# Kernel tuning notes

Hardware: AMD Instinct MI355X
Metric: run time of the kernel (lower is better)

The kernel has to match this reference:

```python
import jax, jax.numpy as jnp
import numpy as np

D_OUT, D1, D2 = 512, 512, 512
R0, R1, R2 = 128, 128, 128
BATCH = 8192


def setup_inputs() -> dict:
    key = jax.random.key(0)
    k1, k2, k3, k4, k5, k6 = jax.random.split(key, 6)
    return {
        "X1": jax.random.normal(k1, (D1, BATCH), dtype=jnp.float32),
        "X2": jax.random.normal(k2, (D2, BATCH), dtype=jnp.float32),
        "U0": jax.random.normal(k3, (D_OUT, R0), dtype=jnp.float32) * 0.05,
        "U1": jax.random.normal(k4, (D1, R1), dtype=jnp.float32) * 0.05,
        "U2": jax.random.normal(k5, (D2, R2), dtype=jnp.float32) * 0.05,
        "G": jax.random.normal(k6, (R0, R1, R2), dtype=jnp.float32) * 0.05,
    }


def reference(X1, X2, U0, U1, U2, G):
    # Per-mode projections: UX_i = U_{i+1}^T @ X_i  -> [r_i, B]
    UX1 = U1.T @ X1  # [R1, B]
    UX2 = U2.T @ X2  # [R2, B]
    # Column-wise Khatri-Rao product of UX1, UX2 gives kron per column with
    # row index q*R2 + r (C order), which matches mode-0 unfolding of G.
    # Fused form: core = G_(0) @ khatri_rao(UX1, UX2), expressed as one einsum.
    core = jnp.einsum('pqr,qb,rb->pb', G, UX1, UX2)  # [R0, B]
    Z = U0 @ core  # [D_OUT, B]
    return Z
```

## Files before the change

### kernel.cpp

```cpp
#include <hip/hip_runtime.h>
#include <hip/hip_bf16.h>
#include <stdint.h>


typedef __attribute__((ext_vector_type(8))) short bf8;
typedef __attribute__((ext_vector_type(4))) short bf4;
typedef __attribute__((ext_vector_type(4))) float f4;

__device__ __forceinline__ unsigned short f2bf(float f){
  unsigned x = __builtin_bit_cast(unsigned, f);
  x += 0x7fffu + ((x >> 16) & 1u);
  return (unsigned short)(x >> 16);
}
__device__ __forceinline__ float bf2f(unsigned short u){
  unsigned x = ((unsigned)u) << 16;
  return __builtin_bit_cast(float, x);
}
__device__ __forceinline__ void glds16(const void* g, void* l){
  __builtin_amdgcn_global_load_lds(
      (const __attribute__((address_space(1))) void*)g,
      (__attribute__((address_space(3))) void*)l, 16, 0, 0);
}

__global__ __launch_bounds__(256) void k_cast(const float* __restrict__ G,
                                              const float* __restrict__ U0,
                                              const float* __restrict__ U1,
                                              const float* __restrict__ U2,
                                              unsigned short* __restrict__ Gbf,
                                              unsigned short* __restrict__ U0bf,
                                              unsigned short* __restrict__ U1T,
                                              unsigned short* __restrict__ U2T){
  const int blk = blockIdx.x;
  if (blk < 2112){
    const int i4 = blk * 256 + threadIdx.x;
    const int NG4 = 2097152 / 4;
    const float4* src; unsigned short* dst; int j4;
    if (i4 < NG4){ src = (const float4*)G;  dst = Gbf;  j4 = i4; }
    else         { src = (const float4*)U0; dst = U0bf; j4 = i4 - NG4; }
    float4 v = src[j4];
    ushort4 o = make_ushort4(f2bf(v.x), f2bf(v.y), f2bf(v.z), f2bf(v.w));
    ((ushort4*)dst)[j4] = o;
  } else {
    const int b2 = blk - 2112;
    const float* U = (b2 < 256) ? U1 : U2;
    unsigned short* UT = (b2 < 256) ? U1T : U2T;
    const int idx = (b2 & 255) * 256 + threadIdx.x;
    const int d = idx >> 7, q = idx & 127;
    UT[q * 512 + d] = f2bf(U[idx]);
  }
}

__global__ __launch_bounds__(256) void k_ux2(const unsigned short* __restrict__ U1T,
                                             const unsigned short* __restrict__ U2T,
                                             const float* __restrict__ X1,
                                             const float* __restrict__ X2,
                                             float* __restrict__ OUTF,
                                             unsigned short* __restrict__ OUTT){
  const bool second = (blockIdx.y != 0);
  const unsigned short* UT = second ? U2T : U1T;
  const float* X = second ? X2 : X1;
  __shared__ __align__(16) unsigned char lds[16384 + 8192];
  unsigned char* ldsA = lds;
  unsigned char* ldsB = lds + 16384;
  const int tid = threadIdx.x, lane = tid & 63, wv = tid >> 6;
  const int wr = wv >> 1, wc = wv & 1;
  const int b0 = blockIdx.x * 64;
  f4 acc[4][2] = {};

  for (int it = 0; it < 8; ++it){
    const int k0 = it * 64;
#pragma unroll
    for (int i = 0; i < 4; ++i){
      const int L = (wv * 4 + i) * 1024 + lane * 16;
      const int row = L >> 7;
      const int ss = (lane & 7) ^ (row & 7);
      glds16(UT + (size_t)row * 512 + k0 + ss * 8, ldsA + (wv * 4 + i) * 1024);
    }
#pragma unroll
    for (int c = 0; c < 2; ++c){
      const int slot = c * 4 + wv;
      const int bRow = lane;
      bf8 v;
#pragma unroll
      for (int j = 0; j < 8; ++j)
        v[j] = (short)f2bf(X[(size_t)(k0 + slot * 8 + j) * 8192 + b0 + bRow]);
      *(bf8*)(ldsB + bRow * 128 + ((slot ^ (bRow & 7)) << 4)) = v;
    }
    __syncthreads();
#pragma unroll
    for (int kc = 0; kc < 2; ++kc){
      const int g = lane >> 4;
      bf8 a[4], b[2];
#pragma unroll
      for (int mf = 0; mf < 4; ++mf){
        const int r = wr * 64 + mf * 16 + (lane & 15);
        a[mf] = *(const bf8*)(ldsA + r * 128 + (((kc * 4 + g) ^ (r & 7)) << 4));
      }
#pragma unroll
      for (int nf = 0; nf < 2; ++nf){
        const int rb = wc * 32 + nf * 16 + (lane & 15);
        b[nf] = *(const bf8*)(ldsB + rb * 128 + (((kc * 4 + g) ^ (rb & 7)) << 4));
      }
#pragma unroll
      for (int mf = 0; mf < 4; ++mf)
#pragma unroll
        for (int nf = 0; nf < 2; ++nf)
          acc[mf][nf] = __builtin_amdgcn_mfma_f32_16x16x32_bf16(a[mf], b[nf], acc[mf][nf], 0, 0, 0);
    }
    __syncthreads();
  }

  if (!second){
#pragma unroll
    for (int mf = 0; mf < 4; ++mf)
#pragma unroll
      for (int nf = 0; nf < 2; ++nf)
#pragma unroll
        for (int j = 0; j < 4; ++j){
          const int q = wr * 64 + mf * 16 + (lane >> 4) * 4 + j;
          const int b = b0 + wc * 32 + nf * 16 + (lane & 15);
          OUTF[(size_t)q * 8192 + b] = acc[mf][nf][j];
        }
  } else {
#pragma unroll
    for (int mf = 0; mf < 4; ++mf)
#pragma unroll
      for (int nf = 0; nf < 2; ++nf){
        const int rBase = wr * 64 + mf * 16 + (lane >> 4) * 4;
        const int bL = wc * 32 + nf * 16 + (lane & 15);
        bf4 p;
#pragma unroll
        for (int j = 0; j < 4; ++j) p[j] = (short)f2bf(acc[mf][nf][j]);
        *(bf4*)(lds + ((bL * 256 + rBase * 2) ^ ((bL & 7) << 4))) = p;
      }
    __syncthreads();
#pragma unroll
    for (int u = 0; u < 4; ++u){
      const int sIdx = u * 256 + tid;
      const int bL = sIdx >> 4, slot = sIdx & 15;
      bf8 v = *(const bf8*)(lds + bL * 256 + ((slot ^ (bL & 7)) << 4));
      *(bf8*)(OUTT + (size_t)(b0 + bL) * 128 + slot * 8) = v;
    }
  }
}

__global__ __launch_bounds__(512, 2) void k_core(const unsigned short* __restrict__ Gbf,
                                                 const float* __restrict__ UX1,
                                                 const unsigned short* __restrict__ UX2T,
                                                 unsigned short* __restrict__ PT){
  __shared__ __align__(16) unsigned char lds[114688];
  unsigned char* ldsX = lds + 98304;
  const int tid = threadIdx.x, lane = tid & 63, wv = tid >> 6;
  const int g = lane >> 4, l15 = lane & 15;
  const int wr = wv >> 2, wc = wv & 3;
  const int blk = blockIdx.x;
  const int split = blk & 7;
  const int b0 = (blk >> 3) * 256;
  const int q0 = split * 16;

  auto stageA = [&](int q, int buf){
#pragma unroll
    for (int rnd = 0; rnd < 4; ++rnd){
      const int off = rnd * 8192 + wv * 1024 + lane * 16;
      const int row = off >> 8;
      const int ss = ((off >> 4) & 15) ^ (row & 7);
      glds16(Gbf + (size_t)row * 16384 + (size_t)q * 128 + ss * 8,
             lds + buf * 32768 + off);
    }
  };

  bf8 Bf[4][4];
#pragma unroll
  for (int kc = 0; kc < 4; ++kc)
#pragma unroll
    for (int nf = 0; nf < 4; ++nf)
      Bf[kc][nf] = *(const bf8*)(UX2T + (size_t)(b0 + wc * 64 + nf * 16 + l15) * 128 +
                                 kc * 32 + g * 8);
#pragma unroll
  for (int rnd = 0; rnd < 2; ++rnd){
    const int off = rnd * 8192 + wv * 1024 + lane * 16;
    const int row = off >> 10;
    glds16(UX1 + (size_t)(q0 + row) * 8192 + b0 + ((off >> 2) & 255), ldsX + off);
  }
  stageA(q0 + 0, 0);
  stageA(q0 + 1, 1);

  f4 acc[4][4];
#pragma unroll
  for (int mf = 0; mf < 4; ++mf)
#pragma unroll
    for (int nf = 0; nf < 4; ++nf) acc[mf][nf] = (f4){0.f, 0.f, 0.f, 0.f};

  int cur = 0;
  for (int i = 0; i < 16; ++i){
    if (i < 15) asm volatile("s_waitcnt vmcnt(4)" ::: "memory");
    else        asm volatile("s_waitcnt vmcnt(0)" ::: "memory");
    __builtin_amdgcn_s_barrier();
    if (i < 14){
      int sbuf = cur + 2; if (sbuf >= 3) sbuf -= 3;
      stageA(q0 + i + 2, sbuf);
    }

    const unsigned char* A = lds + cur * 32768;
    float xs[4];
#pragma unroll
    for (int nf = 0; nf < 4; ++nf)
      xs[nf] = *(const float*)(ldsX + i * 1024 + (wc * 64 + nf * 16 + l15) * 4);
#pragma unroll
    for (int mf = 0; mf < 4; ++mf){
      const int row = wr * 64 + mf * 16 + l15;
      bf8 a[4];
#pragma unroll
      for (int kc = 0; kc < 4; ++kc)
        a[kc] = *(const bf8*)(A + row * 256 + ((((kc << 2) + g) ^ (row & 7)) << 4));
#pragma unroll
      for (int nf = 0; nf < 4; ++nf){
        f4 y = __builtin_amdgcn_mfma_f32_16x16x32_bf16(a[0], Bf[0][nf], (f4){0.f,0.f,0.f,0.f}, 0, 0, 0);
        y = __builtin_amdgcn_mfma_f32_16x16x32_bf16(a[1], Bf[1][nf], y, 0, 0, 0);
        y = __builtin_amdgcn_mfma_f32_16x16x32_bf16(a[2], Bf[2][nf], y, 0, 0, 0);
        y = __builtin_amdgcn_mfma_f32_16x16x32_bf16(a[3], Bf[3][nf], y, 0, 0, 0);
        acc[mf][nf] += y * xs[nf];
      }
    }
    ++cur; if (cur == 3) cur = 0;
  }

  __syncthreads();
#pragma unroll
  for (int mf = 0; mf < 4; ++mf)
#pragma unroll
    for (int nf = 0; nf < 4; ++nf){
      const int bL = wc * 64 + nf * 16 + l15;
      const int pq = wr * 16 + mf * 4 + g;
      bf4 o;
#pragma unroll
      for (int j = 0; j < 4; ++j) o[j] = (short)f2bf(acc[mf][nf][j]);
      *(bf4*)(lds + bL * 256 + ((pq ^ (bL & 7)) << 3)) = o;
    }
  __syncthreads();
#pragma unroll
  for (int rnd = 0; rnd < 8; ++rnd){
    const int idx = rnd * 512 + tid;
    const int bL = idx >> 4, s8 = idx & 15;
    bf4 lo = *(const bf4*)(lds + bL * 256 + (((s8 * 2) ^ (bL & 7)) << 3));
    bf4 hi = *(const bf4*)(lds + bL * 256 + (((s8 * 2 + 1) ^ (bL & 7)) << 3));
    bf8 o;
#pragma unroll
    for (int j = 0; j < 4; ++j){ o[j] = lo[j]; o[4 + j] = hi[j]; }
    *(bf8*)(PT + (size_t)split * 1048576 + (size_t)(b0 + bL) * 128 + s8 * 8) = o;
  }
}

__global__ __launch_bounds__(256) void k_red(const unsigned short* __restrict__ PT,
                                             unsigned short* __restrict__ coreT){
  const int c = blockIdx.x * 256 + threadIdx.x;
  const bf8* P = (const bf8*)PT;
  float s[8] = {};
#pragma unroll
  for (int sp = 0; sp < 8; ++sp){
    bf8 v = P[c + sp * 131072];
#pragma unroll
    for (int j = 0; j < 8; ++j) s[j] += bf2f((unsigned short)v[j]);
  }
  bf8 o;
#pragma unroll
  for (int j = 0; j < 8; ++j) o[j] = (short)f2bf(s[j]);
  ((bf8*)coreT)[c] = o;
}

__global__ __launch_bounds__(256) void k_z(const unsigned short* __restrict__ U0bf,
                                           const unsigned short* __restrict__ coreT,
                                           float* __restrict__ Z){
  __shared__ __align__(16) unsigned char lds[32768];
  unsigned char* ldsA = lds;
  unsigned char* ldsB = lds + 16384;
  const int tid = threadIdx.x, lane = tid & 63, wv = tid >> 6;
  const int wr = wv >> 1, wc = wv & 1;
  const int b0 = blockIdx.x * 128;
  const int d0 = blockIdx.y * 128;
  f4 acc[4][4] = {};

#pragma unroll
  for (int it = 0; it < 2; ++it){
    const int k0 = it * 64;
#pragma unroll
    for (int i = 0; i < 4; ++i){
      const int L = (wv * 4 + i) * 1024 + lane * 16;
      const int row = L >> 7;
      const int ss = (lane & 7) ^ (row & 7);
      glds16(U0bf + (size_t)(d0 + row) * 128 + k0 + ss * 8, ldsA + (wv * 4 + i) * 1024);
      glds16(coreT + (size_t)(b0 + row) * 128 + k0 + ss * 8, ldsB + (wv * 4 + i) * 1024);
    }
    __syncthreads();
#pragma unroll
    for (int kc = 0; kc < 2; ++kc){
      const int g = lane >> 4;
      bf8 a[4], b[4];
#pragma unroll
      for (int mf = 0; mf < 4; ++mf){
        const int r = wr * 64 + mf * 16 + (lane & 15);
        a[mf] = *(const bf8*)(ldsA + r * 128 + (((kc * 4 + g) ^ (r & 7)) << 4));
      }
#pragma unroll
      for (int nf = 0; nf < 4; ++nf){
        const int rb = wc * 64 + nf * 16 + (lane & 15);
        b[nf] = *(const bf8*)(ldsB + rb * 128 + (((kc * 4 + g) ^ (rb & 7)) << 4));
      }
#pragma unroll
      for (int mf = 0; mf < 4; ++mf)
#pragma unroll
        for (int nf = 0; nf < 4; ++nf)
          acc[mf][nf] = __builtin_amdgcn_mfma_f32_16x16x32_bf16(a[mf], b[nf], acc[mf][nf], 0, 0, 0);
    }
    __syncthreads();
  }
#pragma unroll
  for (int mf = 0; mf < 4; ++mf)
#pragma unroll
    for (int nf = 0; nf < 4; ++nf)
#pragma unroll
      for (int j = 0; j < 4; ++j){
        const int d = d0 + wr * 64 + mf * 16 + (lane >> 4) * 4 + j;
        const int b = b0 + wc * 64 + nf * 16 + (lane & 15);
        Z[(size_t)d * 8192 + b] = acc[mf][nf][j];
      }
}

extern "C" void kernel_launch(void* const* d_in, const int* in_sizes, int n_in,
                              void* d_out, int out_size, void* d_ws, size_t ws_size,
                              hipStream_t stream){
  const float* X1 = (const float*)d_in[0];
  const float* X2 = (const float*)d_in[1];
  const float* U0 = (const float*)d_in[2];
  const float* U1 = (const float*)d_in[3];
  const float* U2 = (const float*)d_in[4];
  const float* G  = (const float*)d_in[5];
  float* Z = (float*)d_out;

  char* ws = (char*)d_ws;
  unsigned short* Gbf   = (unsigned short*)(ws);
  unsigned short* U0bf  = (unsigned short*)(ws + 4194304);
  unsigned short* U1T   = (unsigned short*)(ws + 4325376);
  unsigned short* U2T   = (unsigned short*)(ws + 4456448);
  float*          UX1   = (float*)         (ws + 4587520);
  unsigned short* UX2T  = (unsigned short*)(ws + 8781824);
  unsigned short* coreT = (unsigned short*)(ws + 10878976);
  unsigned short* PT    = (unsigned short*)(ws + 12976128);

  k_cast<<<dim3(2624), dim3(256), 0, stream>>>(G, U0, U1, U2, Gbf, U0bf, U1T, U2T);
  k_ux2 <<<dim3(128, 2), dim3(256), 0, stream>>>(U1T, U2T, X1, X2, UX1, UX2T);
  k_core<<<dim3(256), dim3(512), 0, stream>>>(Gbf, UX1, UX2T, PT);
  k_red <<<dim3(512), dim3(256), 0, stream>>>(PT, coreT);
  k_z   <<<dim3(64, 4), dim3(256), 0, stream>>>(U0bf, coreT, Z);
}
```

Measured before the change: 69.11 us.

## Split k_core into smaller blocks with double-buffered G staging and direct stores

k_core now launches 1024 blocks of 256 threads instead of 256 blocks of 512. Each block covers 64 rows of p and 128 batch columns, which cuts LDS use to 32KB and allows more blocks per CU. The triple-buffered pipeline with manual vmcnt waits becomes a simple double buffer with __syncthreads. UX1 scalars are read straight from global memory rather than staged in LDS, and results go directly to PT as 8-byte stores without the LDS transpose. The trade-offs are less latency hiding, more redundant UX2T loads across blocks, and narrower, less coalesced output writes.

```diff
diff --git a/kernel.cpp b/kernel.cpp
--- a/kernel.cpp
+++ b/kernel.cpp
@@ -144,28 +144,31 @@
   }
 }
 
-__global__ __launch_bounds__(512, 2) void k_core(const unsigned short* __restrict__ Gbf,
+__global__ __launch_bounds__(256, 3) void k_core(const unsigned short* __restrict__ Gbf,
                                                  const float* __restrict__ UX1,
                                                  const unsigned short* __restrict__ UX2T,
                                                  unsigned short* __restrict__ PT){
-  __shared__ __align__(16) unsigned char lds[114688];
-  unsigned char* ldsX = lds + 98304;
-  const int tid = threadIdx.x, lane = tid & 63, wv = tid >> 6;
+  __shared__ __align__(16) unsigned char lds[32768];
+  const int tid = threadIdx.x, lane = tid & 63;
+  const int wv = tid >> 6;
   const int g = lane >> 4, l15 = lane & 15;
-  const int wr = wv >> 2, wc = wv & 3;
+  const int wr = wv >> 1, wc = wv & 1;
   const int blk = blockIdx.x;
   const int split = blk & 7;
-  const int b0 = (blk >> 3) * 256;
+  const int rest = blk >> 3;
+  const int pt = (rest & 1) * 64;
+  const int b0 = (rest >> 1) * 128;
   const int q0 = split * 16;
 
   auto stageA = [&](int q, int buf){
 #pragma unroll
     for (int rnd = 0; rnd < 4; ++rnd){
-      const int off = rnd * 8192 + wv * 1024 + lane * 16;
+      const int off = rnd * 4096 + tid * 16;
       const int row = off >> 8;
-      const int ss = ((off >> 4) & 15) ^ (row & 7);
-      glds16(Gbf + (size_t)row * 16384 + (size_t)q * 128 + ss * 8,
-             lds + buf * 32768 + off);
+      const int slot = (off >> 4) & 15;
+      const int ss = slot ^ (row & 15);
+      glds16(Gbf + (size_t)(pt + row) * 16384 + (size_t)q * 128 + ss * 8,
+             lds + buf * 16384 + off);
     }
   };
 
@@ -176,43 +179,30 @@
     for (int nf = 0; nf < 4; ++nf)
       Bf[kc][nf] = *(const bf8*)(UX2T + (size_t)(b0 + wc * 64 + nf * 16 + l15) * 128 +
                                  kc * 32 + g * 8);
-#pragma unroll
-  for (int rnd = 0; rnd < 2; ++rnd){
-    const int off = rnd * 8192 + wv * 1024 + lane * 16;
-    const int row = off >> 10;
-    glds16(UX1 + (size_t)(q0 + row) * 8192 + b0 + ((off >> 2) & 255), ldsX + off);
-  }
-  stageA(q0 + 0, 0);
-  stageA(q0 + 1, 1);
-
-  f4 acc[4][4];
-#pragma unroll
-  for (int mf = 0; mf < 4; ++mf)
+  stageA(q0, 0);
+
+  f4 acc[2][4];
+#pragma unroll
+  for (int mf = 0; mf < 2; ++mf)
 #pragma unroll
     for (int nf = 0; nf < 4; ++nf) acc[mf][nf] = (f4){0.f, 0.f, 0.f, 0.f};
 
-  int cur = 0;
   for (int i = 0; i < 16; ++i){
-    if (i < 15) asm volatile("s_waitcnt vmcnt(4)" ::: "memory");
-    else        asm volatile("s_waitcnt vmcnt(0)" ::: "memory");
-    __builtin_amdgcn_s_barrier();
-    if (i < 14){
-      int sbuf = cur + 2; if (sbuf >= 3) sbuf -= 3;
-      stageA(q0 + i + 2, sbuf);
-    }
-
-    const unsigned char* A = lds + cur * 32768;
+    __syncthreads();
+    if (i < 15) stageA(q0 + i + 1, (i + 1) & 1);
+
+    const unsigned char* A = lds + (i & 1) * 16384;
     float xs[4];
 #pragma unroll
     for (int nf = 0; nf < 4; ++nf)
-      xs[nf] = *(const float*)(ldsX + i * 1024 + (wc * 64 + nf * 16 + l15) * 4);
-#pragma unroll
-    for (int mf = 0; mf < 4; ++mf){
-      const int row = wr * 64 + mf * 16 + l15;
+      xs[nf] = UX1[(size_t)(q0 + i) * 8192 + b0 + wc * 64 + nf * 16 + l15];
+#pragma unroll
+    for (int mf = 0; mf < 2; ++mf){
+      const int row = wr * 32 + mf * 16 + l15;
       bf8 a[4];
 #pragma unroll
       for (int kc = 0; kc < 4; ++kc)
-        a[kc] = *(const bf8*)(A + row * 256 + ((((kc << 2) + g) ^ (row & 7)) << 4));
+        a[kc] = *(const bf8*)(A + row * 256 + ((((kc << 2) + g) ^ l15) << 4));
 #pragma unroll
       for (int nf = 0; nf < 4; ++nf){
         f4 y = __builtin_amdgcn_mfma_f32_16x16x32_bf16(a[0], Bf[0][nf], (f4){0.f,0.f,0.f,0.f}, 0, 0, 0);
@@ -222,33 +212,18 @@
         acc[mf][nf] += y * xs[nf];
       }
     }
-    ++cur; if (cur == 3) cur = 0;
-  }
-
-  __syncthreads();
-#pragma unroll
-  for (int mf = 0; mf < 4; ++mf)
+  }
+
+#pragma unroll
+  for (int mf = 0; mf < 2; ++mf)
 #pragma unroll
     for (int nf = 0; nf < 4; ++nf){
-      const int bL = wc * 64 + nf * 16 + l15;
-      const int pq = wr * 16 + mf * 4 + g;
-      bf4 o;
-#pragma unroll
-      for (int j = 0; j < 4; ++j) o[j] = (short)f2bf(acc[mf][nf][j]);
-      *(bf4*)(lds + bL * 256 + ((pq ^ (bL & 7)) << 3)) = o;
-    }
-  __syncthreads();
-#pragma unroll
-  for (int rnd = 0; rnd < 8; ++rnd){
-    const int idx = rnd * 512 + tid;
-    const int bL = idx >> 4, s8 = idx & 15;
-    bf4 lo = *(const bf4*)(lds + bL * 256 + (((s8 * 2) ^ (bL & 7)) << 3));
-    bf4 hi = *(const bf4*)(lds + bL * 256 + (((s8 * 2 + 1) ^ (bL & 7)) << 3));
-    bf8 o;
-#pragma unroll
-    for (int j = 0; j < 4; ++j){ o[j] = lo[j]; o[4 + j] = hi[j]; }
-    *(bf8*)(PT + (size_t)split * 1048576 + (size_t)(b0 + bL) * 128 + s8 * 8) = o;
-  }
+      const int p = pt + wr * 32 + mf * 16 + g * 4;
+      const int b = b0 + wc * 64 + nf * 16 + l15;
+      ushort4 o = make_ushort4(f2bf(acc[mf][nf][0]), f2bf(acc[mf][nf][1]),
+                               f2bf(acc[mf][nf][2]), f2bf(acc[mf][nf][3]));
+      *(ushort4*)(PT + (size_t)split * 1048576 + (size_t)b * 128 + p) = o;
+    }
 }
 
 __global__ __launch_bounds__(256) void k_red(const unsigned short* __restrict__ PT,
@@ -349,7 +324,7 @@
 
   k_cast<<<dim3(2624), dim3(256), 0, stream>>>(G, U0, U1, U2, Gbf, U0bf, U1T, U2T);
   k_ux2 <<<dim3(128, 2), dim3(256), 0, stream>>>(U1T, U2T, X1, X2, UX1, UX2T);
-  k_core<<<dim3(256), dim3(512), 0, stream>>>(Gbf, UX1, UX2T, PT);
+  k_core<<<dim3(1024), dim3(256), 0, stream>>>(Gbf, UX1, UX2T, PT);
   k_red <<<dim3(512), dim3(256), 0, stream>>>(PT, coreT);
   k_z   <<<dim3(64, 4), dim3(256), 0, stream>>>(U0bf, coreT, Z);
 }
```

New measurement: 74.00 us. +7.1%, slower.

## Fuse split-K reduction into output GEMM kernel, keeping U0 fragments in registers

Applied to the files above, without the earlier changes.

Merges the separate partial-sum reduction kernel into the final U0 @ core GEMM. Each 512-thread block sums the eight bf16 partials for 32 batch columns straight into LDS. Each wave then loads its 64 rows of U0 directly from global memory into registers and computes the full 512-row output for those columns. This drops one kernel launch and the coreT round trip through global memory. The cost is that every block re-reads all of U0 from global or L2 with only 256 blocks, and the output tile per block is narrower.

```diff
diff --git a/kernel.cpp b/kernel.cpp
--- a/kernel.cpp
+++ b/kernel.cpp
@@ -251,77 +251,65 @@
   }
 }
 
-__global__ __launch_bounds__(256) void k_red(const unsigned short* __restrict__ PT,
-                                             unsigned short* __restrict__ coreT){
-  const int c = blockIdx.x * 256 + threadIdx.x;
-  const bf8* P = (const bf8*)PT;
-  float s[8] = {};
-#pragma unroll
-  for (int sp = 0; sp < 8; ++sp){
-    bf8 v = P[c + sp * 131072];
-#pragma unroll
-    for (int j = 0; j < 8; ++j) s[j] += bf2f((unsigned short)v[j]);
-  }
-  bf8 o;
-#pragma unroll
-  for (int j = 0; j < 8; ++j) o[j] = (short)f2bf(s[j]);
-  ((bf8*)coreT)[c] = o;
-}
-
-__global__ __launch_bounds__(256) void k_z(const unsigned short* __restrict__ U0bf,
-                                           const unsigned short* __restrict__ coreT,
-                                           float* __restrict__ Z){
-  __shared__ __align__(16) unsigned char lds[32768];
-  unsigned char* ldsA = lds;
-  unsigned char* ldsB = lds + 16384;
+__global__ __launch_bounds__(512, 1) void k_zred(const unsigned short* __restrict__ U0bf,
+                                                 const unsigned short* __restrict__ PT,
+                                                 float* __restrict__ Z){
+  __shared__ __align__(16) unsigned char ldsB[8192];
   const int tid = threadIdx.x, lane = tid & 63, wv = tid >> 6;
-  const int wr = wv >> 1, wc = wv & 1;
-  const int b0 = blockIdx.x * 128;
-  const int d0 = blockIdx.y * 128;
-  f4 acc[4][4] = {};
-
-#pragma unroll
-  for (int it = 0; it < 2; ++it){
-    const int k0 = it * 64;
-#pragma unroll
-    for (int i = 0; i < 4; ++i){
-      const int L = (wv * 4 + i) * 1024 + lane * 16;
-      const int row = L >> 7;
-      const int ss = (lane & 7) ^ (row & 7);
-      glds16(U0bf + (size_t)(d0 + row) * 128 + k0 + ss * 8, ldsA + (wv * 4 + i) * 1024);
-      glds16(coreT + (size_t)(b0 + row) * 128 + k0 + ss * 8, ldsB + (wv * 4 + i) * 1024);
-    }
-    __syncthreads();
-#pragma unroll
-    for (int kc = 0; kc < 2; ++kc){
-      const int g = lane >> 4;
-      bf8 a[4], b[4];
-#pragma unroll
-      for (int mf = 0; mf < 4; ++mf){
-        const int r = wr * 64 + mf * 16 + (lane & 15);
-        a[mf] = *(const bf8*)(ldsA + r * 128 + (((kc * 4 + g) ^ (r & 7)) << 4));
-      }
-#pragma unroll
-      for (int nf = 0; nf < 4; ++nf){
-        const int rb = wc * 64 + nf * 16 + (lane & 15);
-        b[nf] = *(const bf8*)(ldsB + rb * 128 + (((kc * 4 + g) ^ (rb & 7)) << 4));
-      }
-#pragma unroll
-      for (int mf = 0; mf < 4; ++mf)
-#pragma unroll
-        for (int nf = 0; nf < 4; ++nf)
-          acc[mf][nf] = __builtin_amdgcn_mfma_f32_16x16x32_bf16(a[mf], b[nf], acc[mf][nf], 0, 0, 0);
-    }
-    __syncthreads();
-  }
+  const int g = lane >> 4, l15 = lane & 15;
+  const int b0 = blockIdx.x * 32;
+
+  {
+    const int b = tid >> 4, slot = tid & 15;
+    float s[8] = {0.f, 0.f, 0.f, 0.f, 0.f, 0.f, 0.f, 0.f};
+#pragma unroll
+    for (int sp = 0; sp < 8; ++sp){
+      bf8 v = *(const bf8*)(PT + ((size_t)sp * 8192 + b0 + b) * 128 + slot * 8);
+#pragma unroll
+      for (int j = 0; j < 8; ++j) s[j] += bf2f((unsigned short)v[j]);
+    }
+    bf8 o;
+#pragma unroll
+    for (int j = 0; j < 8; ++j) o[j] = (short)f2bf(s[j]);
+    *(bf8*)(ldsB + b * 256 + ((slot ^ (b & 15)) << 4)) = o;
+  }
+
+  bf8 a[4][4];
 #pragma unroll
   for (int mf = 0; mf < 4; ++mf)
 #pragma unroll
-    for (int nf = 0; nf < 4; ++nf)
+    for (int kc = 0; kc < 4; ++kc)
+      a[mf][kc] = *(const bf8*)(U0bf + (size_t)(wv * 64 + mf * 16 + l15) * 128 +
+                                kc * 32 + g * 8);
+
+  __syncthreads();
+
+  f4 acc[4][2];
+#pragma unroll
+  for (int nf = 0; nf < 2; ++nf){
+    bf8 bfr[4];
+    const int row = nf * 16 + l15;
+#pragma unroll
+    for (int kc = 0; kc < 4; ++kc)
+      bfr[kc] = *(const bf8*)(ldsB + row * 256 + ((((kc << 2) + g) ^ (row & 15)) << 4));
+#pragma unroll
+    for (int mf = 0; mf < 4; ++mf){
+      f4 y = __builtin_amdgcn_mfma_f32_16x16x32_bf16(a[mf][0], bfr[0], (f4){0.f,0.f,0.f,0.f}, 0, 0, 0);
+      y = __builtin_amdgcn_mfma_f32_16x16x32_bf16(a[mf][1], bfr[1], y, 0, 0, 0);
+      y = __builtin_amdgcn_mfma_f32_16x16x32_bf16(a[mf][2], bfr[2], y, 0, 0, 0);
+      y = __builtin_amdgcn_mfma_f32_16x16x32_bf16(a[mf][3], bfr[3], y, 0, 0, 0);
+      acc[mf][nf] = y;
+    }
+  }
+
+#pragma unroll
+  for (int mf = 0; mf < 4; ++mf)
+#pragma unroll
+    for (int nf = 0; nf < 2; ++nf)
 #pragma unroll
       for (int j = 0; j < 4; ++j){
-        const int d = d0 + wr * 64 + mf * 16 + (lane >> 4) * 4 + j;
-        const int b = b0 + wc * 64 + nf * 16 + (lane & 15);
+        const int d = wv * 64 + mf * 16 + g * 4 + j;
+        const int b = b0 + nf * 16 + l15;
         Z[(size_t)d * 8192 + b] = acc[mf][nf][j];
       }
 }
@@ -344,12 +332,10 @@
   unsigned short* U2T   = (unsigned short*)(ws + 4456448);
   float*          UX1   = (float*)         (ws + 4587520);
   unsigned short* UX2T  = (unsigned short*)(ws + 8781824);
-  unsigned short* coreT = (unsigned short*)(ws + 10878976);
   unsigned short* PT    = (unsigned short*)(ws + 12976128);
 
   k_cast<<<dim3(2624), dim3(256), 0, stream>>>(G, U0, U1, U2, Gbf, U0bf, U1T, U2T);
   k_ux2 <<<dim3(128, 2), dim3(256), 0, stream>>>(U1T, U2T, X1, X2, UX1, UX2T);
   k_core<<<dim3(256), dim3(512), 0, stream>>>(Gbf, UX1, UX2T, PT);
-  k_red <<<dim3(512), dim3(256), 0, stream>>>(PT, coreT);
-  k_z   <<<dim3(64, 4), dim3(256), 0, stream>>>(U0bf, coreT, Z);
-}
+  k_zred<<<dim3(256), dim3(512), 0, stream>>>(U0bf, PT, Z);
+}
```

Result: no change. 68.92 us (-0.3%).
